# Kernel tuning notes

Hardware: AMD Instinct MI355X
Metric: run time of the kernel (lower is better)

## Reference

```python
import jax, jax.numpy as jnp
import numpy as np
from jax import lax

HEADS = 4
DIM = 64
GATE_HID = 16


def setup_inputs() -> dict:
    key = jax.random.key(0)
    ks = jax.random.split(key, 12)
    b, c, h, w = 2, DIM, 48, 48
    s = 0.05
    x = jax.random.normal(ks[0], (b, c, h, w), jnp.float32)
    Wqkv = jax.random.normal(ks[1], (3 * c, c), jnp.float32) * s
    bqkv = jax.random.normal(ks[2], (3 * c,), jnp.float32) * s
    Wpos = jax.random.normal(ks[3], (3 * c, 1, 3, 3), jnp.float32) * s
    bpos = jax.random.normal(ks[4], (3 * c,), jnp.float32) * s
    Wg1 = jax.random.normal(ks[5], (GATE_HID, 1), jnp.float32) * 0.5
    bg1 = jax.random.normal(ks[6], (GATE_HID,), jnp.float32) * 0.1
    Wg2 = jax.random.normal(ks[7], (1, GATE_HID), jnp.float32) * 0.5
    bg2 = jax.random.normal(ks[8], (1,), jnp.float32) * 0.1
    Wproj = jax.random.normal(ks[9], (c, c), jnp.float32) * s
    bproj = jax.random.normal(ks[10], (c,), jnp.float32) * s
    return {"x": x, "Wqkv": Wqkv, "bqkv": bqkv, "Wpos": Wpos, "bpos": bpos,
            "Wg1": Wg1, "bg1": bg1, "Wg2": Wg2, "bg2": bg2,
            "Wproj": Wproj, "bproj": bproj}


def _forward(x, Wqkv, bqkv, Wpos, bpos, Wg1, bg1, Wg2, bg2, Wproj, bproj):
    b, c, h, w = x.shape
    n = h * w
    heads = HEADS
    hd = c // heads
    scale = hd ** -0.5
    # qkv 1x1 conv then 3x3 depthwise positional conv
    qkv = jnp.einsum('bchw,oc->bohw', x, Wqkv) + bqkv[None, :, None, None]
    qkv = lax.conv_general_dilated(
        qkv, Wpos, window_strides=(1, 1), padding='SAME',
        feature_group_count=3 * c,
        dimension_numbers=('NCHW', 'OIHW', 'NCHW')) + bpos[None, :, None, None]
    q, k, v = jnp.split(qkv, 3, axis=1)

    def to_heads(t):
        # [b,c,h,w] -> [b,heads,n,hd]
        return t.reshape(b, c, n).transpose(0, 2, 1).reshape(b, n, heads, hd).transpose(0, 2, 1, 3)

    q, k, v = to_heads(q), to_heads(k), to_heads(v)
    attn = jnp.einsum('bhid,bhjd->bhij', q, k) * scale  # [b,heads,n,n]
    prob = jax.nn.softmax(attn, axis=-1)
    entropy = -(prob * jnp.log(jnp.clip(prob, 1e-12))).sum(-1).mean(-1)  # [b,heads]
    # entropy gate: sigmoid(fc2(relu(fc1(e)))) * 0.9 + 0.1
    hgate = jax.nn.relu(entropy[..., None] @ Wg1.T + bg1)  # [b,heads,16]
    ratio = jax.nn.sigmoid(hgate @ Wg2.T + bg2)[..., 0] * 0.9 + 0.1  # [b,heads]
    # dynamic per-(batch,head) top-k along rows via rank threshold
    keep = jnp.clip(jnp.ceil(ratio * n).astype(jnp.int32), 1, n)  # [b,heads]
    sorted_desc = -jnp.sort(-attn, axis=-1)  # [b,heads,n,n]
    idx = jnp.broadcast_to((keep - 1)[:, :, None, None], (b, heads, n, 1))
    thresh = jnp.take_along_axis(sorted_desc, idx, axis=-1)  # [b,heads,n,1]
    sparse = jnp.where(attn >= thresh, attn, -jnp.inf)
    p = jax.nn.softmax(sparse, axis=-1)
    out = jnp.einsum('bhij,bhjd->bhid', p, v)  # [b,heads,n,hd]
    out = out.transpose(0, 2, 1, 3).reshape(b, n, c)
    out = out @ Wproj.T + bproj
    return out.transpose(0, 2, 1).reshape(b, c, h, w)


def reference(x, Wqkv, bqkv, Wpos, bpos, Wg1, bg1, Wg2, bg2, Wproj, bproj):
    return _forward(x, Wqkv, bqkv, Wpos, bpos, Wg1, bg1, Wg2, bg2, Wproj, bproj)
```

## Files before the change

### kernel.cpp

```cpp
#include <hip/hip_runtime.h>
#include <hip/hip_fp16.h>


#define NEG_INF (-__builtin_huge_valf())

typedef _Float16 half8_t __attribute__((ext_vector_type(8)));
typedef float floatx4 __attribute__((ext_vector_type(4)));

__device__ __forceinline__ unsigned h2key(unsigned short u) {
  return (u & 0x8000u) ? (unsigned)((~u) & 0xFFFFu) : (unsigned)(u | 0x8000u);
}
__device__ __forceinline__ float key16_to_float(unsigned k) {
  unsigned short u = (k & 0x8000u) ? (unsigned short)(k & 0x7FFFu)
                                   : (unsigned short)((~k) & 0xFFFFu);
  return __half2float(__ushort_as_half(u));
}

__device__ __forceinline__ float max8(uint4 v, float mx) {
  float2 f0 = __half22float2(*(__half2*)&v.x);
  float2 f1 = __half22float2(*(__half2*)&v.y);
  float2 f2 = __half22float2(*(__half2*)&v.z);
  float2 f3 = __half22float2(*(__half2*)&v.w);
  mx = fmaxf(mx, fmaxf(fmaxf(f0.x, f0.y), fmaxf(f1.x, f1.y)));
  mx = fmaxf(mx, fmaxf(fmaxf(f2.x, f2.y), fmaxf(f3.x, f3.y)));
  return mx;
}

__device__ __forceinline__ uint4 maskExp8(uint4 v, float th, float m,
                                          float& sp) {
  float2 f0 = __half22float2(*(__half2*)&v.x);
  float2 f1 = __half22float2(*(__half2*)&v.y);
  float2 f2 = __half22float2(*(__half2*)&v.z);
  float2 f3 = __half22float2(*(__half2*)&v.w);
  float p0 = (f0.x >= th) ? __expf(f0.x - m) : 0.f;
  float p1 = (f0.y >= th) ? __expf(f0.y - m) : 0.f;
  float p2 = (f1.x >= th) ? __expf(f1.x - m) : 0.f;
  float p3 = (f1.y >= th) ? __expf(f1.y - m) : 0.f;
  float p4 = (f2.x >= th) ? __expf(f2.x - m) : 0.f;
  float p5 = (f2.y >= th) ? __expf(f2.y - m) : 0.f;
  float p6 = (f3.x >= th) ? __expf(f3.x - m) : 0.f;
  float p7 = (f3.y >= th) ? __expf(f3.y - m) : 0.f;
  sp += ((p0 + p1) + (p2 + p3)) + ((p4 + p5) + (p6 + p7));
  uint4 o;
  __half2 h0 = __floats2half2_rn(p0, p1); o.x = *(unsigned*)&h0;
  __half2 h1 = __floats2half2_rn(p2, p3); o.y = *(unsigned*)&h1;
  __half2 h2 = __floats2half2_rn(p4, p5); o.z = *(unsigned*)&h2;
  __half2 h3 = __floats2half2_rn(p6, p7); o.w = *(unsigned*)&h3;
  return o;
}

__global__ __launch_bounds__(256) void k_qkv(const float* __restrict__ x,
                                             const float* __restrict__ W,
                                             const float* __restrict__ bias,
                                             float* __restrict__ out) {
  int blk = blockIdx.x;
  int chunk = blk % 9;
  int o = (blk / 9) % 192;
  int b = blk / (9 * 192);
  int pos = chunk * 256 + threadIdx.x;
  const float* xb = x + b * 64 * 2304 + pos;
  const float* wr = W + o * 64;
  float acc = bias[o];
#pragma unroll
  for (int c = 0; c < 64; c++) acc = fmaf(wr[c], xb[c * 2304], acc);
  out[(b * 192 + o) * 2304 + pos] = acc;
}

__global__ __launch_bounds__(256) void k_dw(const float* __restrict__ qkv,
                                            const float* __restrict__ Wpos,
                                            const float* __restrict__ bpos,
                                            _Float16* __restrict__ q2,
                                            _Float16* __restrict__ k2,
                                            _Float16* __restrict__ vt) {
  int blk = blockIdx.x;
  int chunk = blk % 9;
  int ch = (blk / 9) % 192;
  int b = blk / (9 * 192);
  int pos = chunk * 256 + threadIdx.x;
  int yy = pos / 48, xx = pos % 48;
  const float* in = qkv + (b * 192 + ch) * 2304;
  const float* w = Wpos + ch * 9;
  float acc = bpos[ch];
#pragma unroll
  for (int dy = -1; dy <= 1; dy++) {
    int y2 = yy + dy;
    if ((unsigned)y2 < 48u) {
#pragma unroll
      for (int dx = -1; dx <= 1; dx++) {
        int x2 = xx + dx;
        if ((unsigned)x2 < 48u)
          acc = fmaf(w[(dy + 1) * 3 + (dx + 1)], in[y2 * 48 + x2], acc);
      }
    }
  }
  int sel = ch >> 6;
  int c = ch & 63;
  int head = c >> 4, d = c & 15;
  int bh = b * 4 + head;
  if (sel == 2) {
    vt[((size_t)bh * 16 + d) * 2304 + pos] = (_Float16)acc;
  } else {
    if (sel == 0) acc *= 0.25f;
    size_t idx = (size_t)bh * 2304 + pos;
    _Float16 h1 = (_Float16)acc;
    float r = acc - (float)h1;
    _Float16 h2 = (_Float16)r;
    _Float16* dst = (sel == 0) ? q2 : k2;
    dst[idx * 32 + d] = h1;
    dst[idx * 32 + 16 + d] = h2;
  }
}

template <bool STORE>
__global__ __launch_bounds__(256) void k_ent_t(const _Float16* __restrict__ q2,
                                               const _Float16* __restrict__ k2,
                                               float* __restrict__ ent,
                                               _Float16* __restrict__ lgH) {
  __shared__ __align__(16) _Float16 tBuf[4][16][72];
  __shared__ float mWv[4][16], sWv[4][16], uWv[4][16];

  int blk = blockIdx.x;
  int rowtile = blk % 144;
  int bh = blk / 144;
  int row0 = rowtile * 16;
  int tid = threadIdx.x, lane = tid & 63, wave = tid >> 6;
  int m16 = lane & 15, quad = lane >> 4;

  const half8_t* q2v =
      (const half8_t*)(q2 + ((size_t)bh * 2304 + row0 + m16) * 32);
  half8_t A1 = q2v[quad];
  half8_t zh = {};
  half8_t A2 = (lane < 32) ? A1 : zh;
  const half8_t* kbase = (const half8_t*)(k2 + (size_t)bh * 2304 * 32);

  float mreg[4] = {NEG_INF, NEG_INF, NEG_INF, NEG_INF};
  for (int g = 0; g < 9; g++) {
#pragma unroll
    for (int tt = 0; tt < 4; tt++) {
      int t = g * 4 + tt;
      int col = wave * 576 + t * 16 + m16;
      const half8_t* kk = kbase + (size_t)col * 4;
      half8_t b1 = kk[quad & 1];
      half8_t b2 = kk[2 + (quad & 1)];
      floatx4 acc = {};
      acc = __builtin_amdgcn_mfma_f32_16x16x32_f16(A2, b2, acc, 0, 0, 0);
      acc = __builtin_amdgcn_mfma_f32_16x16x32_f16(A1, b1, acc, 0, 0, 0);
#pragma unroll
      for (int i = 0; i < 4; i++) {
        mreg[i] = fmaxf(mreg[i], acc[i]);
        if (STORE) tBuf[wave][quad * 4 + i][tt * 16 + m16] = (_Float16)acc[i];
      }
    }
    if (STORE) {
      __syncthreads();
      int rb = lane >> 3, seg = lane & 7;
#pragma unroll
      for (int it = 0; it < 2; it++) {
        int rr = it * 8 + rb;
        uint4 vv = *(const uint4*)&tBuf[wave][rr][seg * 8];
        *(uint4*)(lgH + ((size_t)bh * 2304 + row0 + rr) * 2304 + wave * 576 +
                  g * 64 + seg * 8) = vv;
      }
      __syncthreads();
    }
  }
#pragma unroll
  for (int off = 1; off < 16; off <<= 1)
#pragma unroll
    for (int i = 0; i < 4; i++)
      mreg[i] = fmaxf(mreg[i], __shfl_xor(mreg[i], off));
  if (m16 == 0) {
#pragma unroll
    for (int i = 0; i < 4; i++) mWv[wave][quad * 4 + i] = mreg[i];
  }
  __syncthreads();
  float mrow[4];
#pragma unroll
  for (int i = 0; i < 4; i++) {
    int r = quad * 4 + i;
    mrow[i] = fmaxf(fmaxf(mWv[0][r], mWv[1][r]), fmaxf(mWv[2][r], mWv[3][r]));
  }

  float s[4] = {0.f, 0.f, 0.f, 0.f}, u[4] = {0.f, 0.f, 0.f, 0.f};
#pragma unroll 4
  for (int t = 0; t < 36; t++) {
    int col = wave * 576 + t * 16 + m16;
    const half8_t* kk = kbase + (size_t)col * 4;
    half8_t b1 = kk[quad & 1];
    half8_t b2 = kk[2 + (quad & 1)];
    floatx4 acc = {};
    acc = __builtin_amdgcn_mfma_f32_16x16x32_f16(A2, b2, acc, 0, 0, 0);
    acc = __builtin_amdgcn_mfma_f32_16x16x32_f16(A1, b1, acc, 0, 0, 0);
#pragma unroll
    for (int i = 0; i < 4; i++) {
      float z = acc[i] - mrow[i];
      float e = __expf(z);
      s[i] += e;
      u[i] = fmaf(z, e, u[i]);
    }
  }
#pragma unroll
  for (int off = 1; off < 16; off <<= 1) {
#pragma unroll
    for (int i = 0; i < 4; i++) {
      s[i] += __shfl_xor(s[i], off);
      u[i] += __shfl_xor(u[i], off);
    }
  }
  if (m16 == 0) {
#pragma unroll
    for (int i = 0; i < 4; i++) {
      sWv[wave][quad * 4 + i] = s[i];
      uWv[wave][quad * 4 + i] = u[i];
    }
  }
  __syncthreads();
  if (tid < 16) {
    float S = sWv[0][tid] + sWv[1][tid] + sWv[2][tid] + sWv[3][tid];
    float U = uWv[0][tid] + uWv[1][tid] + uWv[2][tid] + uWv[3][tid];
    float er = __logf(S) - U / S;
    er += __shfl_xor(er, 1);
    er += __shfl_xor(er, 2);
    er += __shfl_xor(er, 4);
    er += __shfl_xor(er, 8);
    if (tid == 0) atomicAdd(&ent[bh], er);
  }
}

template <bool CACHED>
__global__ __launch_bounds__(256, 7) void k_attn_t(
    const _Float16* __restrict__ q2, const _Float16* __restrict__ k2,
    const _Float16* __restrict__ vt, const _Float16* __restrict__ lgH,
    const float* __restrict__ ent, const float* __restrict__ Wg1,
    const float* __restrict__ bg1, const float* __restrict__ Wg2,
    const float* __restrict__ bg2, float* __restrict__ oh) {
  __shared__ __align__(16) _Float16 pbuf[4][2320];
  __shared__ float sS[4];
  __shared__ float mShF[4][4];
  __shared__ __align__(16) float redSh[4][64];

  int blk = blockIdx.x;
  int rowblk = blk % 576;
  int bh = blk / 576;
  int row0 = rowblk * 4;
  int tid = threadIdx.x, lane = tid & 63, wave = tid >> 6;

  float eAvg = ent[bh] * (1.f / 2304.f);
  float gacc = bg2[0];
#pragma unroll
  for (int i = 0; i < 16; i++) {
    float h = fmaxf(fmaf(eAvg, Wg1[i], bg1[i]), 0.f);
    gacc = fmaf(h, Wg2[i], gacc);
  }
  float ratio = 0.9f / (1.f + __expf(-gacc)) + 0.1f;
  int kp = (int)ceilf(ratio * 2304.f);
  unsigned keep = (unsigned)min(max(kp, 1), 2304);

  float m;
  uint4* dst4 = (uint4*)pbuf[wave];
  if (CACHED) {
    const uint4* src =
        (const uint4*)(lgH + ((size_t)bh * 2304 + row0 + wave) * 2304);
    float mx = NEG_INF;
#pragma unroll
    for (int it = 0; it < 4; it++) {
      int idx = lane + it * 64;
      uint4 v = src[idx];
      dst4[idx] = v;
      mx = max8(v, mx);
    }
    if (lane < 32) {
      uint4 v = src[256 + lane];
      dst4[256 + lane] = v;
      mx = max8(v, mx);
    }
#pragma unroll
    for (int off = 1; off < 64; off <<= 1) mx = fmaxf(mx, __shfl_xor(mx, off));
    m = mx;
  } else {
    int m16 = lane & 15, quad = lane >> 4;
    const half8_t* q2v =
        (const half8_t*)(q2 + ((size_t)bh * 2304 + row0 + (m16 & 3)) * 32);
    half8_t A1 = q2v[quad];
    half8_t zh = {};
    half8_t A2 = (lane < 32) ? A1 : zh;
    const half8_t* kbase = (const half8_t*)(k2 + (size_t)bh * 2304 * 32);
    float ml[4] = {NEG_INF, NEG_INF, NEG_INF, NEG_INF};
#pragma unroll 4
    for (int t = 0; t < 36; t++) {
      int ct = wave * 36 + t;
      int col = ct * 16 + m16;
      const half8_t* kk = kbase + (size_t)col * 4;
      half8_t b1 = kk[quad & 1];
      half8_t b2 = kk[2 + (quad & 1)];
      floatx4 acc = {};
      acc = __builtin_amdgcn_mfma_f32_16x16x32_f16(A2, b2, acc, 0, 0, 0);
      acc = __builtin_amdgcn_mfma_f32_16x16x32_f16(A1, b1, acc, 0, 0, 0);
      if (lane < 16) {
#pragma unroll
        for (int i = 0; i < 4; i++) {
          pbuf[i][ct * 16 + lane] = (_Float16)acc[i];
          ml[i] = fmaxf(ml[i], acc[i]);
        }
      }
    }
#pragma unroll
    for (int off = 1; off < 16; off <<= 1)
#pragma unroll
      for (int i = 0; i < 4; i++) ml[i] = fmaxf(ml[i], __shfl_xor(ml[i], off));
    if (lane == 0) {
#pragma unroll
      for (int i = 0; i < 4; i++) mShF[wave][i] = ml[i];
    }
    __syncthreads();
    m = fmaxf(fmaxf(mShF[0][wave], mShF[1][wave]),
              fmaxf(mShF[2][wave], mShF[3][wave]));
  }

  float th;
  {
    const unsigned short* prow = (const unsigned short*)pbuf[wave];
    unsigned keys[36];
#pragma unroll
    for (int i = 0; i < 36; i++) keys[i] = h2key(prow[lane + i * 64]);
    unsigned T = 0u;
    for (int bit = 15; bit >= 0; --bit) {
      unsigned cand = T | (1u << bit);
      unsigned cnt = 0u;
#pragma unroll
      for (int i = 0; i < 36; i++)
        cnt += (unsigned)__popcll(__ballot(keys[i] >= cand));
      if (cnt >= keep) {
        T = cand;
        if (cnt == keep) break;
      }
    }
    th = key16_to_float(T);
  }

  {
    float sp = 0.f;
#pragma unroll
    for (int it = 0; it < 4; it++) {
      int idx = lane + it * 64;
      dst4[idx] = maskExp8(dst4[idx], th, m, sp);
    }
    if (lane < 32) {
      int idx = 256 + lane;
      dst4[idx] = maskExp8(dst4[idx], th, m, sp);
    }
#pragma unroll
    for (int off = 1; off < 64; off <<= 1) sp += __shfl_xor(sp, off);
    if (lane == 0) sS[wave] = sp;
  }
  __syncthreads();

  {
    int m16 = lane & 15, quad = lane >> 4;
    const _Float16* vrow = vt + ((size_t)bh * 16 + m16) * 2304;
    const _Float16* prow = pbuf[m16 & 3];
    int jb0 = wave * 576 + quad * 8;
    floatx4 acc = {};
#pragma unroll 6
    for (int t = 0; t < 18; t++) {
      int jb = jb0 + t * 32;
      half8_t a = *(const half8_t*)&prow[jb];
      half8_t b = *(const half8_t*)&vrow[jb];
      acc = __builtin_amdgcn_mfma_f32_16x16x32_f16(a, b, acc, 0, 0, 0);
    }
    if (lane < 16) {
      *(floatx4*)&redSh[wave][m16 * 4] = acc;
    }
  }
  __syncthreads();
  if (tid < 64) {
    int r = tid & 3, d = tid >> 2;
    float s2 = redSh[0][d * 4 + r] + redSh[1][d * 4 + r] +
               redSh[2][d * 4 + r] + redSh[3][d * 4 + r];
    oh[((size_t)(bh * 2304 + row0 + r)) * 16 + d] = s2 / sS[r];
  }
}

__global__ __launch_bounds__(256) void k_proj(const float* __restrict__ oh,
                                              const float* __restrict__ Wp,
                                              const float* __restrict__ bp,
                                              float* __restrict__ out) {
  int blk = blockIdx.x;
  int chunk = blk % 9;
  int co = (blk / 9) % 64;
  int b = blk / (9 * 64);
  int pos = chunk * 256 + threadIdx.x;
  const float* wr = Wp + co * 64;
  float acc = bp[co];
#pragma unroll
  for (int head = 0; head < 4; head++) {
    const float4* op =
        (const float4*)(oh + ((size_t)((b * 4 + head) * 2304 + pos)) * 16);
#pragma unroll
    for (int p = 0; p < 4; p++) {
      float4 o4 = op[p];
      acc = fmaf(wr[head * 16 + p * 4 + 0], o4.x, acc);
      acc = fmaf(wr[head * 16 + p * 4 + 1], o4.y, acc);
      acc = fmaf(wr[head * 16 + p * 4 + 2], o4.z, acc);
      acc = fmaf(wr[head * 16 + p * 4 + 3], o4.w, acc);
    }
  }
  out[(b * 64 + co) * 2304 + pos] = acc;
}

extern "C" void kernel_launch(void* const* d_in, const int* in_sizes, int n_in,
                              void* d_out, int out_size, void* d_ws,
                              size_t ws_size, hipStream_t stream) {
  const float* x    = (const float*)d_in[0];
  const float* Wqkv = (const float*)d_in[1];
  const float* bqkv = (const float*)d_in[2];
  const float* Wpos = (const float*)d_in[3];
  const float* bpos = (const float*)d_in[4];
  const float* Wg1  = (const float*)d_in[5];
  const float* bg1  = (const float*)d_in[6];
  const float* Wg2  = (const float*)d_in[7];
  const float* bg2  = (const float*)d_in[8];
  const float* Wpr  = (const float*)d_in[9];
  const float* bpr  = (const float*)d_in[10];
  float* out = (float*)d_out;

  const size_t lgBytes = (size_t)8 * 2304 * 2304 * 2;
  const size_t baseBytes = (size_t)(884736 + 294912 + 8) * 4 +
                           (size_t)(2 * 589824 + 294912) * 2;
  bool cached = ws_size >= lgBytes + baseBytes;

  char* base = (char*)d_ws;
  _Float16* lgH = nullptr;
  if (cached) {
    lgH = (_Float16*)base;
    base += lgBytes;
  }
  float* qkv_raw = (float*)base;
  float* oh = qkv_raw + 884736;
  float* ent = oh + 294912;
  _Float16* q2 = (_Float16*)(ent + 8);
  _Float16* k2 = q2 + 589824;
  _Float16* vt = k2 + 589824;

  (void)hipMemsetAsync(ent, 0, 8 * sizeof(float), stream);
  hipLaunchKernelGGL(k_qkv, dim3(2 * 192 * 9), dim3(256), 0, stream,
                     x, Wqkv, bqkv, qkv_raw);
  hipLaunchKernelGGL(k_dw, dim3(2 * 192 * 9), dim3(256), 0, stream,
                     qkv_raw, Wpos, bpos, q2, k2, vt);
  if (cached) {
    hipLaunchKernelGGL((k_ent_t<true>), dim3(8 * 144), dim3(256), 0, stream,
                       q2, k2, ent, lgH);
    hipLaunchKernelGGL((k_attn_t<true>), dim3(8 * 576), dim3(256), 0, stream,
                       q2, k2, vt, lgH, ent, Wg1, bg1, Wg2, bg2, oh);
  } else {
    hipLaunchKernelGGL((k_ent_t<false>), dim3(8 * 144), dim3(256), 0, stream,
                       q2, k2, ent, lgH);
    hipLaunchKernelGGL((k_attn_t<false>), dim3(8 * 576), dim3(256), 0, stream,
                       q2, k2, vt, lgH, ent, Wg1, bg1, Wg2, bg2, oh);
  }
  hipLaunchKernelGGL(k_proj, dim3(2 * 64 * 9), dim3(256), 0, stream,
                     oh, Wpr, bpr, out);
}
```

Measured before the change: 229.2 us.

## Drop cached logit matrix and recompute 16-row tiles in attention kernel

Removes the path that wrote the full fp16 score matrix to workspace in the entropy pass and read it back in the attention pass. The attention kernel now recomputes QK^T with MFMA for a 16-row tile per 512-thread block, shared by 8 waves, instead of 4 rows per block. This avoids about 85 MB of global write plus read traffic per call. In exchange the dot products are computed twice, LDS use per block rises to about 74 KB, and the output reduction now uses shared-memory atomics.

```diff
diff --git a/kernel.cpp b/kernel.cpp
--- a/kernel.cpp
+++ b/kernel.cpp
@@ -14,16 +14,6 @@
   unsigned short u = (k & 0x8000u) ? (unsigned short)(k & 0x7FFFu)
                                    : (unsigned short)((~k) & 0xFFFFu);
   return __half2float(__ushort_as_half(u));
-}
-
-__device__ __forceinline__ float max8(uint4 v, float mx) {
-  float2 f0 = __half22float2(*(__half2*)&v.x);
-  float2 f1 = __half22float2(*(__half2*)&v.y);
-  float2 f2 = __half22float2(*(__half2*)&v.z);
-  float2 f3 = __half22float2(*(__half2*)&v.w);
-  mx = fmaxf(mx, fmaxf(fmaxf(f0.x, f0.y), fmaxf(f1.x, f1.y)));
-  mx = fmaxf(mx, fmaxf(fmaxf(f2.x, f2.y), fmaxf(f3.x, f3.y)));
-  return mx;
 }
 
 __device__ __forceinline__ uint4 maskExp8(uint4 v, float th, float m,
@@ -111,12 +101,9 @@
   }
 }
 
-template <bool STORE>
-__global__ __launch_bounds__(256) void k_ent_t(const _Float16* __restrict__ q2,
-                                               const _Float16* __restrict__ k2,
-                                               float* __restrict__ ent,
-                                               _Float16* __restrict__ lgH) {
-  __shared__ __align__(16) _Float16 tBuf[4][16][72];
+__global__ __launch_bounds__(256) void k_ent(const _Float16* __restrict__ q2,
+                                             const _Float16* __restrict__ k2,
+                                             float* __restrict__ ent) {
   __shared__ float mWv[4][16], sWv[4][16], uWv[4][16];
 
   int blk = blockIdx.x;
@@ -134,35 +121,17 @@
   const half8_t* kbase = (const half8_t*)(k2 + (size_t)bh * 2304 * 32);
 
   float mreg[4] = {NEG_INF, NEG_INF, NEG_INF, NEG_INF};
-  for (int g = 0; g < 9; g++) {
-#pragma unroll
-    for (int tt = 0; tt < 4; tt++) {
-      int t = g * 4 + tt;
-      int col = wave * 576 + t * 16 + m16;
-      const half8_t* kk = kbase + (size_t)col * 4;
-      half8_t b1 = kk[quad & 1];
-      half8_t b2 = kk[2 + (quad & 1)];
-      floatx4 acc = {};
-      acc = __builtin_amdgcn_mfma_f32_16x16x32_f16(A2, b2, acc, 0, 0, 0);
-      acc = __builtin_amdgcn_mfma_f32_16x16x32_f16(A1, b1, acc, 0, 0, 0);
-#pragma unroll
-      for (int i = 0; i < 4; i++) {
-        mreg[i] = fmaxf(mreg[i], acc[i]);
-        if (STORE) tBuf[wave][quad * 4 + i][tt * 16 + m16] = (_Float16)acc[i];
-      }
-    }
-    if (STORE) {
-      __syncthreads();
-      int rb = lane >> 3, seg = lane & 7;
-#pragma unroll
-      for (int it = 0; it < 2; it++) {
-        int rr = it * 8 + rb;
-        uint4 vv = *(const uint4*)&tBuf[wave][rr][seg * 8];
-        *(uint4*)(lgH + ((size_t)bh * 2304 + row0 + rr) * 2304 + wave * 576 +
-                  g * 64 + seg * 8) = vv;
-      }
-      __syncthreads();
-    }
+#pragma unroll 4
+  for (int t = 0; t < 36; t++) {
+    int col = wave * 576 + t * 16 + m16;
+    const half8_t* kk = kbase + (size_t)col * 4;
+    half8_t b1 = kk[quad & 1];
+    half8_t b2 = kk[2 + (quad & 1)];
+    floatx4 acc = {};
+    acc = __builtin_amdgcn_mfma_f32_16x16x32_f16(A2, b2, acc, 0, 0, 0);
+    acc = __builtin_amdgcn_mfma_f32_16x16x32_f16(A1, b1, acc, 0, 0, 0);
+#pragma unroll
+    for (int i = 0; i < 4; i++) mreg[i] = fmaxf(mreg[i], acc[i]);
   }
 #pragma unroll
   for (int off = 1; off < 16; off <<= 1)
@@ -227,23 +196,26 @@
   }
 }
 
-template <bool CACHED>
-__global__ __launch_bounds__(256, 7) void k_attn_t(
+__global__ __launch_bounds__(512, 4) void k_attn(
     const _Float16* __restrict__ q2, const _Float16* __restrict__ k2,
-    const _Float16* __restrict__ vt, const _Float16* __restrict__ lgH,
-    const float* __restrict__ ent, const float* __restrict__ Wg1,
-    const float* __restrict__ bg1, const float* __restrict__ Wg2,
-    const float* __restrict__ bg2, float* __restrict__ oh) {
-  __shared__ __align__(16) _Float16 pbuf[4][2320];
-  __shared__ float sS[4];
-  __shared__ float mShF[4][4];
-  __shared__ __align__(16) float redSh[4][64];
+    const _Float16* __restrict__ vt, const float* __restrict__ ent,
+    const float* __restrict__ Wg1, const float* __restrict__ bg1,
+    const float* __restrict__ Wg2, const float* __restrict__ bg2,
+    float* __restrict__ oh) {
+  __shared__ __align__(16) _Float16 pbuf[16][2312];
+  __shared__ float mWv[8][16];
+  __shared__ float mFin[16];
+  __shared__ float sS[16];
+  __shared__ float outAcc[16][16];
 
   int blk = blockIdx.x;
-  int rowblk = blk % 576;
-  int bh = blk / 576;
-  int row0 = rowblk * 4;
+  int rowtile = blk % 144;
+  int bh = blk / 144;
+  int row0 = rowtile * 16;
   int tid = threadIdx.x, lane = tid & 63, wave = tid >> 6;
+  int m16 = lane & 15, quad = lane >> 4;
+
+  if (tid < 256) ((float*)outAcc)[tid] = 0.f;
 
   float eAvg = ent[bh] * (1.f / 2304.f);
   float gacc = bg2[0];
@@ -256,39 +228,18 @@
   int kp = (int)ceilf(ratio * 2304.f);
   unsigned keep = (unsigned)min(max(kp, 1), 2304);
 
-  float m;
-  uint4* dst4 = (uint4*)pbuf[wave];
-  if (CACHED) {
-    const uint4* src =
-        (const uint4*)(lgH + ((size_t)bh * 2304 + row0 + wave) * 2304);
-    float mx = NEG_INF;
-#pragma unroll
-    for (int it = 0; it < 4; it++) {
-      int idx = lane + it * 64;
-      uint4 v = src[idx];
-      dst4[idx] = v;
-      mx = max8(v, mx);
-    }
-    if (lane < 32) {
-      uint4 v = src[256 + lane];
-      dst4[256 + lane] = v;
-      mx = max8(v, mx);
-    }
-#pragma unroll
-    for (int off = 1; off < 64; off <<= 1) mx = fmaxf(mx, __shfl_xor(mx, off));
-    m = mx;
-  } else {
-    int m16 = lane & 15, quad = lane >> 4;
+  {
     const half8_t* q2v =
-        (const half8_t*)(q2 + ((size_t)bh * 2304 + row0 + (m16 & 3)) * 32);
+        (const half8_t*)(q2 + ((size_t)bh * 2304 + row0 + m16) * 32);
     half8_t A1 = q2v[quad];
     half8_t zh = {};
     half8_t A2 = (lane < 32) ? A1 : zh;
     const half8_t* kbase = (const half8_t*)(k2 + (size_t)bh * 2304 * 32);
-    float ml[4] = {NEG_INF, NEG_INF, NEG_INF, NEG_INF};
-#pragma unroll 4
-    for (int t = 0; t < 36; t++) {
-      int ct = wave * 36 + t;
+
+    float mreg[4] = {NEG_INF, NEG_INF, NEG_INF, NEG_INF};
+#pragma unroll 3
+    for (int t = 0; t < 18; t++) {
+      int ct = wave * 18 + t;
       int col = ct * 16 + m16;
       const half8_t* kk = kbase + (size_t)col * 4;
       half8_t b1 = kk[quad & 1];
@@ -296,88 +247,94 @@
       floatx4 acc = {};
       acc = __builtin_amdgcn_mfma_f32_16x16x32_f16(A2, b2, acc, 0, 0, 0);
       acc = __builtin_amdgcn_mfma_f32_16x16x32_f16(A1, b1, acc, 0, 0, 0);
-      if (lane < 16) {
-#pragma unroll
-        for (int i = 0; i < 4; i++) {
-          pbuf[i][ct * 16 + lane] = (_Float16)acc[i];
-          ml[i] = fmaxf(ml[i], acc[i]);
+#pragma unroll
+      for (int i = 0; i < 4; i++) {
+        mreg[i] = fmaxf(mreg[i], acc[i]);
+        pbuf[quad * 4 + i][col] = (_Float16)acc[i];
+      }
+    }
+#pragma unroll
+    for (int off = 1; off < 16; off <<= 1)
+#pragma unroll
+      for (int i = 0; i < 4; i++)
+        mreg[i] = fmaxf(mreg[i], __shfl_xor(mreg[i], off));
+    if (m16 == 0) {
+#pragma unroll
+      for (int i = 0; i < 4; i++) mWv[wave][quad * 4 + i] = mreg[i];
+    }
+  }
+  __syncthreads();
+  if (tid < 16) {
+    float mm = mWv[0][tid];
+#pragma unroll
+    for (int w = 1; w < 8; w++) mm = fmaxf(mm, mWv[w][tid]);
+    mFin[tid] = mm;
+  }
+  __syncthreads();
+
+#pragma unroll
+  for (int rr = 0; rr < 2; rr++) {
+    int r = wave * 2 + rr;
+    float m = mFin[r];
+    float th;
+    {
+      const unsigned short* prow = (const unsigned short*)pbuf[r];
+      unsigned keys[36];
+#pragma unroll
+      for (int i = 0; i < 36; i++) keys[i] = h2key(prow[lane + i * 64]);
+      unsigned T = 0u;
+      for (int bit = 15; bit >= 0; --bit) {
+        unsigned cand = T | (1u << bit);
+        unsigned cnt = 0u;
+#pragma unroll
+        for (int i = 0; i < 36; i++)
+          cnt += (unsigned)__popcll(__ballot(keys[i] >= cand));
+        if (cnt >= keep) {
+          T = cand;
+          if (cnt == keep) break;
         }
       }
-    }
-#pragma unroll
-    for (int off = 1; off < 16; off <<= 1)
-#pragma unroll
-      for (int i = 0; i < 4; i++) ml[i] = fmaxf(ml[i], __shfl_xor(ml[i], off));
-    if (lane == 0) {
-#pragma unroll
-      for (int i = 0; i < 4; i++) mShF[wave][i] = ml[i];
-    }
-    __syncthreads();
-    m = fmaxf(fmaxf(mShF[0][wave], mShF[1][wave]),
-              fmaxf(mShF[2][wave], mShF[3][wave]));
-  }
-
-  float th;
+      th = key16_to_float(T);
+    }
+    {
+      uint4* prow4 = (uint4*)pbuf[r];
+      float sp = 0.f;
+#pragma unroll
+      for (int it = 0; it < 4; it++) {
+        int idx = lane + it * 64;
+        prow4[idx] = maskExp8(prow4[idx], th, m, sp);
+      }
+      if (lane < 32) {
+        int idx = 256 + lane;
+        prow4[idx] = maskExp8(prow4[idx], th, m, sp);
+      }
+#pragma unroll
+      for (int off = 1; off < 64; off <<= 1) sp += __shfl_xor(sp, off);
+      if (lane == 0) sS[r] = sp;
+    }
+  }
+  __syncthreads();
+
   {
-    const unsigned short* prow = (const unsigned short*)pbuf[wave];
-    unsigned keys[36];
-#pragma unroll
-    for (int i = 0; i < 36; i++) keys[i] = h2key(prow[lane + i * 64]);
-    unsigned T = 0u;
-    for (int bit = 15; bit >= 0; --bit) {
-      unsigned cand = T | (1u << bit);
-      unsigned cnt = 0u;
-#pragma unroll
-      for (int i = 0; i < 36; i++)
-        cnt += (unsigned)__popcll(__ballot(keys[i] >= cand));
-      if (cnt >= keep) {
-        T = cand;
-        if (cnt == keep) break;
-      }
-    }
-    th = key16_to_float(T);
-  }
-
-  {
-    float sp = 0.f;
-#pragma unroll
-    for (int it = 0; it < 4; it++) {
-      int idx = lane + it * 64;
-      dst4[idx] = maskExp8(dst4[idx], th, m, sp);
-    }
-    if (lane < 32) {
-      int idx = 256 + lane;
-      dst4[idx] = maskExp8(dst4[idx], th, m, sp);
-    }
-#pragma unroll
-    for (int off = 1; off < 64; off <<= 1) sp += __shfl_xor(sp, off);
-    if (lane == 0) sS[wave] = sp;
-  }
-  __syncthreads();
-
-  {
-    int m16 = lane & 15, quad = lane >> 4;
     const _Float16* vrow = vt + ((size_t)bh * 16 + m16) * 2304;
-    const _Float16* prow = pbuf[m16 & 3];
-    int jb0 = wave * 576 + quad * 8;
+    const _Float16* prow = pbuf[m16];
+    int jb0 = wave * 288 + quad * 8;
     floatx4 acc = {};
-#pragma unroll 6
-    for (int t = 0; t < 18; t++) {
+#pragma unroll 3
+    for (int t = 0; t < 9; t++) {
       int jb = jb0 + t * 32;
       half8_t a = *(const half8_t*)&prow[jb];
       half8_t b = *(const half8_t*)&vrow[jb];
       acc = __builtin_amdgcn_mfma_f32_16x16x32_f16(a, b, acc, 0, 0, 0);
     }
-    if (lane < 16) {
-      *(floatx4*)&redSh[wave][m16 * 4] = acc;
-    }
-  }
-  __syncthreads();
-  if (tid < 64) {
-    int r = tid & 3, d = tid >> 2;
-    float s2 = redSh[0][d * 4 + r] + redSh[1][d * 4 + r] +
-               redSh[2][d * 4 + r] + redSh[3][d * 4 + r];
-    oh[((size_t)(bh * 2304 + row0 + r)) * 16 + d] = s2 / sS[r];
+#pragma unroll
+    for (int i = 0; i < 4; i++)
+      atomicAdd(&outAcc[quad * 4 + i][m16], acc[i]);
+  }
+  __syncthreads();
+  if (tid < 256) {
+    int r = tid >> 4, d = tid & 15;
+    oh[((size_t)(bh * 2304 + row0 + r)) * 16 + d] = outAcc[r][d] / sS[r];
   }
 }
 
@@ -424,18 +381,7 @@
   const float* bpr  = (const float*)d_in[10];
   float* out = (float*)d_out;
 
-  const size_t lgBytes = (size_t)8 * 2304 * 2304 * 2;
-  const size_t baseBytes = (size_t)(884736 + 294912 + 8) * 4 +
-                           (size_t)(2 * 589824 + 294912) * 2;
-  bool cached = ws_size >= lgBytes + baseBytes;
-
-  char* base = (char*)d_ws;
-  _Float16* lgH = nullptr;
-  if (cached) {
-    lgH = (_Float16*)base;
-    base += lgBytes;
-  }
-  float* qkv_raw = (float*)base;
+  float* qkv_raw = (float*)d_ws;
   float* oh = qkv_raw + 884736;
   float* ent = oh + 294912;
   _Float16* q2 = (_Float16*)(ent + 8);
@@ -447,17 +393,10 @@
                      x, Wqkv, bqkv, qkv_raw);
   hipLaunchKernelGGL(k_dw, dim3(2 * 192 * 9), dim3(256), 0, stream,
                      qkv_raw, Wpos, bpos, q2, k2, vt);
-  if (cached) {
-    hipLaunchKernelGGL((k_ent_t<true>), dim3(8 * 144), dim3(256), 0, stream,
-                       q2, k2, ent, lgH);
-    hipLaunchKernelGGL((k_attn_t<true>), dim3(8 * 576), dim3(256), 0, stream,
-                       q2, k2, vt, lgH, ent, Wg1, bg1, Wg2, bg2, oh);
-  } else {
-    hipLaunchKernelGGL((k_ent_t<false>), dim3(8 * 144), dim3(256), 0, stream,
-                       q2, k2, ent, lgH);
-    hipLaunchKernelGGL((k_attn_t<false>), dim3(8 * 576), dim3(256), 0, stream,
-                       q2, k2, vt, lgH, ent, Wg1, bg1, Wg2, bg2, oh);
-  }
+  hipLaunchKernelGGL(k_ent, dim3(8 * 144), dim3(256), 0, stream,
+                     q2, k2, ent);
+  hipLaunchKernelGGL(k_attn, dim3(8 * 144), dim3(512), 0, stream,
+                     q2, k2, vt, ent, Wg1, bg1, Wg2, bg2, oh);
   hipLaunchKernelGGL(k_proj, dim3(2 * 64 * 9), dim3(256), 0, stream,
                      oh, Wpr, bpr, out);
 }
```

Result: slower. 266.0 us (+16.0%).
